# Kernel tuning notes

Measured on AMD Instinct MI355X. Metric: run time of the kernel, lower is better.

The kernel has to match this reference:

```python
import jax, jax.numpy as jnp
import numpy as np

EPS = 1e-8  # matches torch F.cosine_similarity default eps


def _flatten_spatial(x):
    # [B, C, d, h, w] -> [B, N, C]
    B, C = x.shape[:2]
    return x.reshape(B, C, -1).transpose(0, 2, 1)


def _stage_loss(canon_src, canon_tgt, src_desc, tgt_desc):
    stage_size = src_desc.shape[2:]
    B, C = canon_src.shape[:2]
    # trilinear resize with half-pixel centers == torch align_corners=False
    rs = jax.image.resize(canon_src, (B, C) + stage_size, method='trilinear')
    rt = jax.image.resize(canon_tgt, (B, C) + stage_size, method='trilinear')
    a = _flatten_spatial(rs)  # [B, N, 3]
    b = _flatten_spatial(rt)  # [B, N, 3]
    # squared euclidean distances (argmin is invariant to sqrt)
    a2 = jnp.sum(a * a, axis=-1)  # [B, N]
    b2 = jnp.sum(b * b, axis=-1)  # [B, N]
    ab = jnp.einsum('bnc,bmc->bnm', a, b)  # [B, N, N]
    d2 = a2[:, :, None] + b2[:, None, :] - 2.0 * ab
    nearest = jnp.argmin(d2, axis=-1)  # [B, N] int
    sd = _flatten_spatial(src_desc)  # [B, N, Cd]
    td = _flatten_spatial(tgt_desc)  # [B, N, Cd]
    gathered = jnp.take_along_axis(td, nearest[:, :, None], axis=1)  # [B, N, Cd]
    num = jnp.sum(sd * gathered, axis=-1)
    denom = jnp.maximum(jnp.linalg.norm(sd, axis=-1), EPS) * \
            jnp.maximum(jnp.linalg.norm(gathered, axis=-1), EPS)
    cos = num / denom
    return 1.0 - jnp.mean(cos)


def setup_inputs() -> dict:
    key = jax.random.key(0)
    ks = jax.random.split(key, 6)
    return {
        'canonical_source': jax.random.normal(ks[0], (4, 3, 64, 64, 64), jnp.float32),
        'canonical_target': jax.random.normal(ks[1], (4, 3, 64, 64, 64), jnp.float32),
        'src_desc0': jax.random.normal(ks[2], (4, 32, 16, 16, 16), jnp.float32),
        'tgt_desc0': jax.random.normal(ks[3], (4, 32, 16, 16, 16), jnp.float32),
        'src_desc1': jax.random.normal(ks[4], (4, 32, 8, 8, 8), jnp.float32),
        'tgt_desc1': jax.random.normal(ks[5], (4, 32, 8, 8, 8), jnp.float32),
    }


def reference(canonical_source, canonical_target, src_desc0, tgt_desc0, src_desc1, tgt_desc1):
    l0 = _stage_loss(canonical_source, canonical_target, src_desc0, tgt_desc0)
    l1 = _stage_loss(canonical_source, canonical_target, src_desc1, tgt_desc1)
    return jnp.stack([l0, l1]).mean()
```

## Files before the change

kernel.cpp:

```cpp
#include <hip/hip_runtime.h>
#include <cfloat>

typedef unsigned long long u64;

#define CDESC 32
#define N0 4096
#define N1 512

__device__ __forceinline__ unsigned fbits_mono(float d) {
    unsigned b = __float_as_uint(d);
    return (d >= 0.f) ? (b | 0x80000000u) : ~b;
}

__device__ __forceinline__ void wave_reduce_atomic(float v, float* acc) {
#pragma unroll
    for (int off = 32; off > 0; off >>= 1) v += __shfl_down(v, off, 64);
    if ((threadIdx.x & 63) == 0) atomicAdd(acc, v);
}

__global__ __launch_bounds__(256) void pass1_fused(
        const float* __restrict__ csrc, const float* __restrict__ ctgt,
        const float* __restrict__ sd0, const float* __restrict__ td0,
        const float* __restrict__ sd1, const float* __restrict__ td1,
        float* __restrict__ t16a, float* __restrict__ t16b,
        float* __restrict__ t8a,  float* __restrict__ t8b,
        float* __restrict__ sd0T, float* __restrict__ td0T,
        float* __restrict__ sd1T, float* __restrict__ td1T,
        float* __restrict__ acc) {
    __shared__ __align__(16) float sRow[4096];
    const int tid = threadIdx.x;
    const int bx  = blockIdx.x, by = blockIdx.y;
    if (by == 0 && bx == 0 && tid < 4) acc[tid] = 0.f;

    if (bx < 768) {
        int bc = bx >> 6, z = bx & 63;
        const float* in = by ? ctgt : csrc;
        float* o16 = by ? t16b : t16a;
        float* o8  = by ? t8b  : t8a;
        const float4* src = (const float4*)(in + (size_t)(bc * 64 + z) * 4096);
        float4* dst = (float4*)sRow;
#pragma unroll
        for (int k = 0; k < 4; ++k)
            dst[tid + k * 256] = src[tid + k * 256];
        __syncthreads();
#pragma unroll
        for (int k = 0; k < 6; ++k) {
            int o = tid + k * 256;
            if (o < 1024) {
                int y = o >> 4, xo = o & 15;
                int j0 = 4 * xo - 2;
                float sum = 0.f, wsum = 0.f;
#pragma unroll
                for (int t = 0; t < 8; ++t) {
                    int j = j0 + t;
                    float w = 1.f - fabsf((float)t - 3.5f) / 4.f;
                    if (j >= 0 && j < 64) { sum = fmaf(w, sRow[y * 64 + j], sum); wsum += w; }
                }
                o16[bc * 65536 + z * 1024 + y * 16 + xo] = sum / wsum;
            } else {
                int o2 = o - 1024;
                int y = o2 >> 3, xo = o2 & 7;
                int j0 = 8 * xo - 4;
                float sum = 0.f, wsum = 0.f;
#pragma unroll
                for (int t = 0; t < 16; ++t) {
                    int j = j0 + t;
                    float w = 1.f - fabsf((float)t - 7.5f) / 8.f;
                    if (j >= 0 && j < 64) { sum = fmaf(w, sRow[y * 64 + j], sum); wsum += w; }
                }
                o8[bc * 32768 + z * 512 + y * 8 + xo] = sum / wsum;
            }
        }
    } else {
        __shared__ float tile[64 * 33];
        int tl = bx - 768;
        const float* din; float* dout; int N, b, n0;
        if (tl < 256) { din = by ? td0 : sd0; dout = by ? td0T : sd0T;
                        N = N0; b = tl >> 6; n0 = (tl & 63) * 64; }
        else { tl -= 256; din = by ? td1 : sd1; dout = by ? td1T : sd1T;
               N = N1; b = tl >> 3; n0 = (tl & 7) * 64; }
#pragma unroll
        for (int i = 0; i < 8; ++i) {
            int idx = tid + i * 256;
            int c = idx >> 6, j = idx & 63;
            tile[j * 33 + c] = din[((size_t)b * CDESC + c) * N + n0 + j];
        }
        __syncthreads();
#pragma unroll
        for (int i = 0; i < 8; ++i) {
            int idx = tid + i * 256;
            int p = idx >> 5, c = idx & 31;
            dout[((size_t)b * N + n0 + p) * CDESC + c] = tile[p * 33 + c];
        }
    }
}

__global__ __launch_bounds__(256) void pass2_both(
        const float* __restrict__ t16a, const float* __restrict__ t16b,
        const float* __restrict__ t8a,  const float* __restrict__ t8b,
        float4* __restrict__ ps0, float4* __restrict__ pt0,
        float4* __restrict__ ps1, float4* __restrict__ pt1) {
    int gid = blockIdx.x * 256 + threadIdx.x;
    if (blockIdx.x < 1024) {
        int sub = gid & 7, p = gid >> 3;
        int side = p >> 14, r = p & 16383;
        int b = r >> 12, n = r & 4095;
        int x = n & 15, y = (n >> 4) & 15, z = n >> 8;
        const float* t = side ? t16b : t16a;
        float wy[8]; int jy[8];
        float wys = 0.f, wzs = 0.f;
#pragma unroll
        for (int tt = 0; tt < 8; ++tt) {
            float w = 1.f - fabsf((float)tt - 3.5f) * 0.25f;
            int j = 4 * y - 2 + tt;
            bool v = (unsigned)j < 64u;
            wy[tt] = v ? w : 0.f; jy[tt] = v ? j : 0; wys += wy[tt];
            int jz = 4 * z - 2 + tt;
            if ((unsigned)jz < 64u) wzs += w;
        }
        float a0 = 0.f, a1 = 0.f, a2 = 0.f;
        {
            float wz = 1.f - fabsf((float)sub - 3.5f) * 0.25f;
            int jz = 4 * z - 2 + sub;
            if ((unsigned)jz < 64u) {
                const float* bz = t + (size_t)b * 196608 + jz * 1024 + x;
#pragma unroll
                for (int ty = 0; ty < 8; ++ty) {
                    float w = wz * wy[ty];
                    const float* pr = bz + jy[ty] * 16;
                    a0 = fmaf(w, pr[0],      a0);
                    a1 = fmaf(w, pr[65536],  a1);
                    a2 = fmaf(w, pr[131072], a2);
                }
            }
        }
#pragma unroll
        for (int m = 1; m < 8; m <<= 1) {
            a0 += __shfl_xor(a0, m, 64);
            a1 += __shfl_xor(a1, m, 64);
            a2 += __shfl_xor(a2, m, 64);
        }
        if (sub == 0) {
            float inv = 1.f / (wys * wzs);
            a0 *= inv; a1 *= inv; a2 *= inv;
            float4* pts = side ? pt0 : ps0;
            pts[b * N0 + n] = make_float4(a0, a1, a2, a0 * a0 + a1 * a1 + a2 * a2);
        }
    } else {
        int g = gid - 262144;
        int sub = g & 7, p = g >> 3;
        int side = p >> 11, r = p & 2047;
        int b = r >> 9, n = r & 511;
        int x = n & 7, y = (n >> 3) & 7, z = n >> 6;
        const float* t = side ? t8b : t8a;
        constexpr int CS = 64 * 64 * 8;
        float wy[16]; int jy[16];
        float wys = 0.f, wzs = 0.f;
#pragma unroll
        for (int tt = 0; tt < 16; ++tt) {
            float w = 1.f - fabsf((float)tt - 7.5f) * 0.125f;
            int j = 8 * y - 4 + tt;
            bool v = (unsigned)j < 64u;
            wy[tt] = v ? w : 0.f; jy[tt] = v ? j : 0; wys += wy[tt];
            int jz = 8 * z - 4 + tt;
            if ((unsigned)jz < 64u) wzs += w;
        }
        float a0 = 0.f, a1 = 0.f, a2 = 0.f;
#pragma unroll
        for (int k = 0; k < 2; ++k) {
            int tt = 2 * sub + k;
            float wz = 1.f - fabsf((float)tt - 7.5f) * 0.125f;
            int jz = 8 * z - 4 + tt;
            if ((unsigned)jz < 64u) {
                const float* bz = t + b * 3 * CS + jz * (64 * 8) + x;
#pragma unroll 1
                for (int ty = 0; ty < 16; ++ty) {
                    float w = wz * wy[ty];
                    const float* pr = bz + jy[ty] * 8;
                    a0 = fmaf(w, pr[0],      a0);
                    a1 = fmaf(w, pr[CS],     a1);
                    a2 = fmaf(w, pr[2 * CS], a2);
                }
            }
        }
#pragma unroll
        for (int m = 1; m < 8; m <<= 1) {
            a0 += __shfl_xor(a0, m, 64);
            a1 += __shfl_xor(a1, m, 64);
            a2 += __shfl_xor(a2, m, 64);
        }
        if (sub == 0) {
            float inv = 1.f / (wys * wzs);
            a0 *= inv; a1 *= inv; a2 *= inv;
            float4* pts = side ? pt1 : ps1;
            pts[b * N1 + n] = make_float4(a0, a1, a2, a0 * a0 + a1 * a1 + a2 * a2);
        }
    }
}

__device__ __forceinline__ float cos_pm(const float* __restrict__ sT,
                                        const float* __restrict__ tT,
                                        size_t si, size_t ti) {
    const float4* s = (const float4*)(sT + si * CDESC);
    const float4* t = (const float4*)(tT + ti * CDESC);
    float num = 0.f, s2 = 0.f, t2 = 0.f;
#pragma unroll
    for (int c = 0; c < 8; ++c) {
        float4 a = s[c], g = t[c];
        num = fmaf(a.x, g.x, fmaf(a.y, g.y, fmaf(a.z, g.z, fmaf(a.w, g.w, num))));
        s2  = fmaf(a.x, a.x, fmaf(a.y, a.y, fmaf(a.z, a.z, fmaf(a.w, a.w, s2))));
        t2  = fmaf(g.x, g.x, fmaf(g.y, g.y, fmaf(g.z, g.z, fmaf(g.w, g.w, t2))));
    }
    return num / (fmaxf(sqrtf(s2), 1e-8f) * fmaxf(sqrtf(t2), 1e-8f));
}

__global__ __launch_bounds__(256) void nn_cos_all(
        const float4* __restrict__ ps0, const float4* __restrict__ pt0,
        const float* __restrict__ sd0T, const float* __restrict__ td0T,
        const float4* __restrict__ ps1, const float4* __restrict__ pt1,
        const float* __restrict__ sd1T, const float* __restrict__ td1T,
        float* acc, float* __restrict__ out) {
    extern __shared__ __align__(16) char smraw[];
    float4* sm = (float4*)smraw;
    const int tid = threadIdx.x;
    const int bx  = blockIdx.x;

    if (bx < 256) {
        int b = bx >> 6, ptile = bx & 63;
        const float4* tp = pt0 + b * N0;
        for (int i = tid; i < N0; i += 256) {
            float4 q = tp[i];
            sm[i] = make_float4(-2.f * q.x, -2.f * q.y, -2.f * q.z, q.w);
        }
        __syncthreads();
        int w = tid >> 6, lane = tid & 63;
        int n = ptile * 64 + lane;
        float4 P = ps0[b * N0 + n];
        float best = FLT_MAX; int bi = 0;
        const int m0 = w * 1024;
#pragma unroll 16
        for (int k = 0; k < 1024; ++k) {
            float4 Q = sm[m0 + k];
            float d = fmaf(P.x, Q.x, fmaf(P.y, Q.y, fmaf(P.z, Q.z, Q.w)));
            if (d < best) { best = d; bi = k; }
        }
        u64 key = ((u64)fbits_mono(best) << 32) | (unsigned)(m0 + bi);
        __syncthreads();
        u64* keys = (u64*)smraw;
        keys[w * 64 + lane] = key;
        __syncthreads();
        if (tid < 64) {
            u64 k0 = keys[tid],       k1 = keys[tid + 64];
            u64 k2 = keys[tid + 128], k3 = keys[tid + 192];
            u64 ka = k0 < k1 ? k0 : k1;
            u64 kb = k2 < k3 ? k2 : k3;
            u64 kk = ka < kb ? ka : kb;
            int nearest = (int)(unsigned)(kk & 0xFFFFFFFFull);
            int n2 = ptile * 64 + tid;
            float cosv = cos_pm(sd0T, td0T, (size_t)b * N0 + n2,
                                (size_t)b * N0 + nearest);
            wave_reduce_atomic(cosv, acc + 0);
        }
    } else {
        int bb = bx - 256;
        int b = bb >> 1;
        const float4* tp = pt1 + b * N1;
        for (int i = tid; i < N1; i += 256) {
            float4 qq = tp[i];
            sm[i] = make_float4(-2.f * qq.x, -2.f * qq.y, -2.f * qq.z, qq.w);
        }
        __syncthreads();
        int n = (bb & 1) * 256 + tid;
        float4 P = ps1[b * N1 + n];
        float best = FLT_MAX; int bi = 0;
#pragma unroll 16
        for (int m = 0; m < N1; ++m) {
            float4 Q = sm[m];
            float d = fmaf(P.x, Q.x, fmaf(P.y, Q.y, fmaf(P.z, Q.z, Q.w)));
            if (d < best) { best = d; bi = m; }
        }
        float cosv = cos_pm(sd1T, td1T, (size_t)b * N1 + n, (size_t)b * N1 + bi);
        wave_reduce_atomic(cosv, acc + 1);
    }

    __syncthreads();
    if (tid == 0) {
        __threadfence();
        unsigned old = atomicAdd((unsigned*)(acc + 2), 1u);
        if (old == 263u) {
            float a0 = atomicAdd(acc + 0, 0.f);
            float a1 = atomicAdd(acc + 1, 0.f);
            out[0] = 1.f - 0.5f * (a0 * (1.f / 16384.f) + a1 * (1.f / 2048.f));
        }
    }
}

extern "C" void kernel_launch(void* const* d_in, const int* in_sizes, int n_in,
                              void* d_out, int out_size, void* d_ws, size_t ws_size,
                              hipStream_t stream) {
    const float* c_src = (const float*)d_in[0];
    const float* c_tgt = (const float*)d_in[1];
    const float* sd0   = (const float*)d_in[2];
    const float* td0   = (const float*)d_in[3];
    const float* sd1   = (const float*)d_in[4];
    const float* td1   = (const float*)d_in[5];
    float* out = (float*)d_out;

    char* ws = (char*)d_ws;
    float* acc  = (float*)ws;
    float* t16a = (float*)(ws + 256);
    float* t16b = t16a + 786432;
    float* t8a  = t16b + 786432;
    float* t8b  = t8a + 393216;
    float4* ps0 = (float4*)(t8b + 393216);
    float4* pt0 = ps0 + 16384;
    float4* ps1 = pt0 + 16384;
    float4* pt1 = ps1 + 2048;
    float* sd0T = (float*)(pt1 + 2048);
    float* td0T = sd0T + 524288;
    float* sd1T = td0T + 524288;
    float* td1T = sd1T + 65536;

    pass1_fused<<<dim3(1056, 2), 256, 0, stream>>>(c_src, c_tgt, sd0, td0, sd1, td1,
                                                   t16a, t16b, t8a, t8b,
                                                   sd0T, td0T, sd1T, td1T, acc);
    pass2_both<<<1152, 256, 0, stream>>>(t16a, t16b, t8a, t8b, ps0, pt0, ps1, pt1);
    nn_cos_all<<<264, 256, 65536, stream>>>(ps0, pt0, sd0T, td0T, ps1, pt1,
                                            sd1T, td1T, acc, out);
}
```

Baseline: 129.0 us.

## Use blocked fminf argmin, prescale targets upstream, and pad resize smem rows

The nearest-neighbour scan now computes 16 distances per block, reduces them with a fminf tree, and only tracks the block base. A second pass over the winning block recovers the exact index, replacing a compare-and-select per candidate with cheaper min ops. The -2 scaling of target points moves into the producing kernel so the consumer does a plain copy into shared memory. The resize kernel's shared row buffer gets stride 65 to avoid bank conflicts. The recompute-and-equality step relies on identical FMA evaluation so tie-breaking stays first-index.

```diff
diff --git a/kernel.cpp b/kernel.cpp
--- a/kernel.cpp
+++ b/kernel.cpp
@@ -27,7 +27,7 @@
         float* __restrict__ sd0T, float* __restrict__ td0T,
         float* __restrict__ sd1T, float* __restrict__ td1T,
         float* __restrict__ acc) {
-    __shared__ __align__(16) float sRow[4096];
+    __shared__ __align__(16) float sRow[65 * 64];
     const int tid = threadIdx.x;
     const int bx  = blockIdx.x, by = blockIdx.y;
     if (by == 0 && bx == 0 && tid < 4) acc[tid] = 0.f;
@@ -38,10 +38,14 @@
         float* o16 = by ? t16b : t16a;
         float* o8  = by ? t8b  : t8a;
         const float4* src = (const float4*)(in + (size_t)(bc * 64 + z) * 4096);
-        float4* dst = (float4*)sRow;
-#pragma unroll
-        for (int k = 0; k < 4; ++k)
-            dst[tid + k * 256] = src[tid + k * 256];
+#pragma unroll
+        for (int k = 0; k < 4; ++k) {
+            float4 v = src[tid + k * 256];
+            int g = tid + k * 256;
+            int y = g >> 4, j = (g & 15) * 4;
+            float* p = &sRow[y * 65 + j];
+            p[0] = v.x; p[1] = v.y; p[2] = v.z; p[3] = v.w;
+        }
         __syncthreads();
 #pragma unroll
         for (int k = 0; k < 6; ++k) {
@@ -54,7 +58,7 @@
                 for (int t = 0; t < 8; ++t) {
                     int j = j0 + t;
                     float w = 1.f - fabsf((float)t - 3.5f) / 4.f;
-                    if (j >= 0 && j < 64) { sum = fmaf(w, sRow[y * 64 + j], sum); wsum += w; }
+                    if (j >= 0 && j < 64) { sum = fmaf(w, sRow[y * 65 + j], sum); wsum += w; }
                 }
                 o16[bc * 65536 + z * 1024 + y * 16 + xo] = sum / wsum;
             } else {
@@ -66,7 +70,7 @@
                 for (int t = 0; t < 16; ++t) {
                     int j = j0 + t;
                     float w = 1.f - fabsf((float)t - 7.5f) / 8.f;
-                    if (j >= 0 && j < 64) { sum = fmaf(w, sRow[y * 64 + j], sum); wsum += w; }
+                    if (j >= 0 && j < 64) { sum = fmaf(w, sRow[y * 65 + j], sum); wsum += w; }
                 }
                 o8[bc * 32768 + z * 512 + y * 8 + xo] = sum / wsum;
             }
@@ -143,8 +147,9 @@
         if (sub == 0) {
             float inv = 1.f / (wys * wzs);
             a0 *= inv; a1 *= inv; a2 *= inv;
-            float4* pts = side ? pt0 : ps0;
-            pts[b * N0 + n] = make_float4(a0, a1, a2, a0 * a0 + a1 * a1 + a2 * a2);
+            float sq = a0 * a0 + a1 * a1 + a2 * a2;
+            if (side) pt0[b * N0 + n] = make_float4(-2.f * a0, -2.f * a1, -2.f * a2, sq);
+            else      ps0[b * N0 + n] = make_float4(a0, a1, a2, sq);
         }
     } else {
         int g = gid - 262144;
@@ -192,8 +197,9 @@
         if (sub == 0) {
             float inv = 1.f / (wys * wzs);
             a0 *= inv; a1 *= inv; a2 *= inv;
-            float4* pts = side ? pt1 : ps1;
-            pts[b * N1 + n] = make_float4(a0, a1, a2, a0 * a0 + a1 * a1 + a2 * a2);
+            float sq = a0 * a0 + a1 * a1 + a2 * a2;
+            if (side) pt1[b * N1 + n] = make_float4(-2.f * a0, -2.f * a1, -2.f * a2, sq);
+            else      ps1[b * N1 + n] = make_float4(a0, a1, a2, sq);
         }
     }
 }
@@ -212,6 +218,10 @@
         t2  = fmaf(g.x, g.x, fmaf(g.y, g.y, fmaf(g.z, g.z, fmaf(g.w, g.w, t2))));
     }
     return num / (fmaxf(sqrtf(s2), 1e-8f) * fmaxf(sqrtf(t2), 1e-8f));
+}
+
+__device__ __forceinline__ float dist_pm(float4 P, float4 Q) {
+    return fmaf(P.x, Q.x, fmaf(P.y, Q.y, fmaf(P.z, Q.z, Q.w)));
 }
 
 __global__ __launch_bounds__(256) void nn_cos_all(
@@ -228,23 +238,35 @@
     if (bx < 256) {
         int b = bx >> 6, ptile = bx & 63;
         const float4* tp = pt0 + b * N0;
-        for (int i = tid; i < N0; i += 256) {
-            float4 q = tp[i];
-            sm[i] = make_float4(-2.f * q.x, -2.f * q.y, -2.f * q.z, q.w);
-        }
+        for (int i = tid; i < N0; i += 256)
+            sm[i] = tp[i];
         __syncthreads();
         int w = tid >> 6, lane = tid & 63;
         int n = ptile * 64 + lane;
         float4 P = ps0[b * N0 + n];
-        float best = FLT_MAX; int bi = 0;
         const int m0 = w * 1024;
-#pragma unroll 16
-        for (int k = 0; k < 1024; ++k) {
-            float4 Q = sm[m0 + k];
-            float d = fmaf(P.x, Q.x, fmaf(P.y, Q.y, fmaf(P.z, Q.z, Q.w)));
-            if (d < best) { best = d; bi = k; }
-        }
-        u64 key = ((u64)fbits_mono(best) << 32) | (unsigned)(m0 + bi);
+        float best = FLT_MAX; int bbase = 0;
+        for (int k0 = 0; k0 < 1024; k0 += 16) {
+            float d[16];
+#pragma unroll
+            for (int u = 0; u < 16; ++u)
+                d[u] = dist_pm(P, sm[m0 + k0 + u]);
+            float e0 = fminf(d[0],  d[1]),  e1 = fminf(d[2],  d[3]);
+            float e2 = fminf(d[4],  d[5]),  e3 = fminf(d[6],  d[7]);
+            float e4 = fminf(d[8],  d[9]),  e5 = fminf(d[10], d[11]);
+            float e6 = fminf(d[12], d[13]), e7 = fminf(d[14], d[15]);
+            float f0 = fminf(e0, e1), f1 = fminf(e2, e3);
+            float f2 = fminf(e4, e5), f3 = fminf(e6, e7);
+            float bm = fminf(fminf(f0, f1), fminf(f2, f3));
+            if (bm < best) { best = bm; bbase = k0; }
+        }
+        int bi = 0;
+#pragma unroll
+        for (int u = 15; u >= 0; --u) {
+            float dv = dist_pm(P, sm[m0 + bbase + u]);
+            if (dv == best) bi = u;
+        }
+        u64 key = ((u64)fbits_mono(best) << 32) | (unsigned)(m0 + bbase + bi);
         __syncthreads();
         u64* keys = (u64*)smraw;
         keys[w * 64 + lane] = key;
@@ -265,21 +287,34 @@
         int bb = bx - 256;
         int b = bb >> 1;
         const float4* tp = pt1 + b * N1;
-        for (int i = tid; i < N1; i += 256) {
-            float4 qq = tp[i];
-            sm[i] = make_float4(-2.f * qq.x, -2.f * qq.y, -2.f * qq.z, qq.w);
-        }
+        for (int i = tid; i < N1; i += 256)
+            sm[i] = tp[i];
         __syncthreads();
         int n = (bb & 1) * 256 + tid;
         float4 P = ps1[b * N1 + n];
-        float best = FLT_MAX; int bi = 0;
-#pragma unroll 16
-        for (int m = 0; m < N1; ++m) {
-            float4 Q = sm[m];
-            float d = fmaf(P.x, Q.x, fmaf(P.y, Q.y, fmaf(P.z, Q.z, Q.w)));
-            if (d < best) { best = d; bi = m; }
-        }
-        float cosv = cos_pm(sd1T, td1T, (size_t)b * N1 + n, (size_t)b * N1 + bi);
+        float best = FLT_MAX; int bbase = 0;
+        for (int k0 = 0; k0 < N1; k0 += 16) {
+            float d[16];
+#pragma unroll
+            for (int u = 0; u < 16; ++u)
+                d[u] = dist_pm(P, sm[k0 + u]);
+            float e0 = fminf(d[0],  d[1]),  e1 = fminf(d[2],  d[3]);
+            float e2 = fminf(d[4],  d[5]),  e3 = fminf(d[6],  d[7]);
+            float e4 = fminf(d[8],  d[9]),  e5 = fminf(d[10], d[11]);
+            float e6 = fminf(d[12], d[13]), e7 = fminf(d[14], d[15]);
+            float f0 = fminf(e0, e1), f1 = fminf(e2, e3);
+            float f2 = fminf(e4, e5), f3 = fminf(e6, e7);
+            float bm = fminf(fminf(f0, f1), fminf(f2, f3));
+            if (bm < best) { best = bm; bbase = k0; }
+        }
+        int bi = 0;
+#pragma unroll
+        for (int u = 15; u >= 0; --u) {
+            float dv = dist_pm(P, sm[bbase + u]);
+            if (dv == best) bi = u;
+        }
+        float cosv = cos_pm(sd1T, td1T, (size_t)b * N1 + n,
+                            (size_t)b * N1 + bbase + bi);
         wave_reduce_atomic(cosv, acc + 1);
     }
 
```

Measured after the change: 125.3 us. 1.03x faster.
